# Kernel tuning notes

Hardware: AMD Instinct MI355X
Metric: run time of the kernel (lower is better)

## Reference

```python
import jax, jax.numpy as jnp
from jax import lax
import numpy as np

WIN = 9
PAD = WIN // 2  # 4 -> SAME output size
SIM_FACTOR = 1.0
REG_FACTOR = 0.1
EPS = 1e-5

_DN = ('NCHW', 'OIHW', 'NCHW')


def box_sum(x):
    """9x9 sliding-window sum via two separable 1D ones-convs (same math as a 9x9 ones conv2d)."""
    kh = jnp.ones((1, 1, WIN, 1), x.dtype)
    kw = jnp.ones((1, 1, 1, WIN), x.dtype)
    y = lax.conv_general_dilated(x, kh, (1, 1), [(PAD, PAD), (0, 0)], dimension_numbers=_DN)
    return lax.conv_general_dilated(y, kw, (1, 1), [(0, 0), (PAD, PAD)], dimension_numbers=_DN)


def ncc2d(Ii, Ji):
    win_size = float(WIN * WIN)
    I_sum = box_sum(Ii)
    J_sum = box_sum(Ji)
    I2_sum = box_sum(Ii * Ii)
    J2_sum = box_sum(Ji * Ji)
    IJ_sum = box_sum(Ii * Ji)
    u_I = I_sum / win_size
    u_J = J_sum / win_size
    cross = IJ_sum - u_J * I_sum - u_I * J_sum + u_I * u_J * win_size
    I_var = I2_sum - 2.0 * u_I * I_sum + u_I * u_I * win_size
    J_var = J2_sum - 2.0 * u_J * J_sum + u_J * u_J * win_size
    cc = cross * cross / (I_var * J_var + EPS)
    return -jnp.mean(cc)


def grad2d_l2(y_pred):
    dy = y_pred[:, :, 1:, :] - y_pred[:, :, :-1, :]
    dx = y_pred[:, :, :, 1:] - y_pred[:, :, :, :-1]
    return (jnp.mean(dx * dx) + jnp.mean(dy * dy)) / 2.0


def setup_inputs() -> dict:
    key = jax.random.key(0)
    k1, k2, k3 = jax.random.split(key, 3)
    B, H, W = 64, 512, 512
    return {
        'target_proj': jax.random.uniform(k1, (B, 1, H, W), dtype=jnp.float32),
        'warped_moving': jax.random.uniform(k2, (B, 1, H, W), dtype=jnp.float32),
        'phi': jax.random.normal(k3, (B, 2, H, W), dtype=jnp.float32),
    }


def reference(target_proj, warped_moving, phi):
    loss_sim = ncc2d(target_proj, warped_moving) * SIM_FACTOR
    loss_reg = grad2d_l2(phi) * REG_FACTOR
    total = loss_sim + loss_reg
    return (loss_sim, loss_reg, total)
```

## Files before the change

kernel.cpp:

```cpp
#include <hip/hip_runtime.h>

#define HH 512
#define WW 512
#define RSTRIP 16
#define NCC_BLOCKS 512
#define REG_BLOCKS 512

__device__ __forceinline__ void ldrow8(const float* __restrict__ row, int lane,
                                       float v[8]) {
    const float4* p = reinterpret_cast<const float4*>(row) + (lane << 1);
    float4 a = p[0], b = p[1];
    v[0] = a.x; v[1] = a.y; v[2] = a.z; v[3] = a.w;
    v[4] = b.x; v[5] = b.y; v[6] = b.z; v[7] = b.w;
}

__device__ __forceinline__ void fold(const float d[8], int lane, float* B) {
    float hl0 = __shfl_up(d[4], 1), hl1 = __shfl_up(d[5], 1);
    float hl2 = __shfl_up(d[6], 1), hl3 = __shfl_up(d[7], 1);
    float hr0 = __shfl_down(d[0], 1), hr1 = __shfl_down(d[1], 1);
    float hr2 = __shfl_down(d[2], 1), hr3 = __shfl_down(d[3], 1);
    hl0 = lane ? hl0 : 0.f; hl1 = lane ? hl1 : 0.f;
    hl2 = lane ? hl2 : 0.f; hl3 = lane ? hl3 : 0.f;
    bool nr = (lane != 63);
    hr0 = nr ? hr0 : 0.f; hr1 = nr ? hr1 : 0.f;
    hr2 = nr ? hr2 : 0.f; hr3 = nr ? hr3 : 0.f;

    float s = ((hl0 + hl1) + (hl2 + hl3)) +
              ((d[0] + d[1]) + (d[2] + d[3])) + d[4];
    B[0] += s;
    s += d[5] - hl0;  B[1] += s;
    s += d[6] - hl1;  B[2] += s;
    s += d[7] - hl2;  B[3] += s;
    s += hr0 - hl3;   B[4] += s;
    s += hr1 - d[0];  B[5] += s;
    s += hr2 - d[1];  B[6] += s;
    s += hr3 - d[2];  B[7] += s;
}

template<bool HASL, bool HAST>
__device__ __forceinline__ void upd8(const float* __restrict__ Il,
                                     const float* __restrict__ Jl,
                                     const float* __restrict__ It,
                                     const float* __restrict__ Jt,
                                     int lane, float B[5][8]) {
    float LI[8], LJ[8], TI[8], TJ[8], d[8];
    if (HASL) { ldrow8(Il, lane, LI); ldrow8(Jl, lane, LJ); }
    if (HAST) { ldrow8(It, lane, TI); ldrow8(Jt, lane, TJ); }

#pragma unroll
    for (int c = 0; c < 8; ++c)
        d[c] = HASL ? (HAST ? LI[c] - TI[c] : LI[c]) : -TI[c];
    fold(d, lane, B[0]);
#pragma unroll
    for (int c = 0; c < 8; ++c)
        d[c] = HASL ? (HAST ? LJ[c] - TJ[c] : LJ[c]) : -TJ[c];
    fold(d, lane, B[1]);
#pragma unroll
    for (int c = 0; c < 8; ++c)
        d[c] = HASL ? (HAST ? fmaf(LI[c], LI[c], -(TI[c] * TI[c]))
                            : LI[c] * LI[c])
                    : -(TI[c] * TI[c]);
    fold(d, lane, B[2]);
#pragma unroll
    for (int c = 0; c < 8; ++c)
        d[c] = HASL ? (HAST ? fmaf(LJ[c], LJ[c], -(TJ[c] * TJ[c]))
                            : LJ[c] * LJ[c])
                    : -(TJ[c] * TJ[c]);
    fold(d, lane, B[3]);
#pragma unroll
    for (int c = 0; c < 8; ++c)
        d[c] = HASL ? (HAST ? fmaf(LI[c], LJ[c], -(TI[c] * TJ[c]))
                            : LI[c] * LJ[c])
                    : -(TI[c] * TJ[c]);
    fold(d, lane, B[4]);
}

__device__ void ncc_body(int sbid, const float* __restrict__ I,
                         const float* __restrict__ J, float* __restrict__ ws,
                         float* sh) {
    const int T = threadIdx.x;
    const int lane = T & 63;
    const int strip = (sbid << 2) | (T >> 6);
    const int b = strip >> 5;
    const int s = strip & 31;
    const int r0 = s << 4;

    const float* Ib = I + (size_t)b * (HH * WW);
    const float* Jb = J + (size_t)b * (HH * WW);

    float B[5][8];
#pragma unroll
    for (int k = 0; k < 5; ++k)
#pragma unroll
        for (int o = 0; o < 8; ++o) B[k][o] = 0.f;

    for (int j = r0 - 4; j <= r0 + 4; ++j) {
        if (j >= 0)
            upd8<true, false>(Ib + (size_t)j * WW, Jb + (size_t)j * WW,
                              Ib, Jb, lane, B);
    }

    const float inv81 = 1.f / 81.f;
    float acc = 0.f;
    for (int h = 0;; ++h) {
#pragma unroll
        for (int o = 0; o < 8; ++o) {
            float IS = B[0][o], JS = B[1][o];
            float I2 = B[2][o], J2 = B[3][o], IJ = B[4][o];
            float cross = fmaf(-(IS * JS), inv81, IJ);
            float Iv = fmaf(-(IS * IS), inv81, I2);
            float Jv = fmaf(-(JS * JS), inv81, J2);
            float denom = fmaf(Iv, Jv, 1e-5f);
            acc = fmaf(cross * cross, __builtin_amdgcn_rcpf(denom), acc);
        }
        if (h == RSTRIP - 1) break;
        const int jl = r0 + h + 5;
        const int jt = r0 + h - 4;
        const float* IlP = Ib + (size_t)jl * WW;
        const float* JlP = Jb + (size_t)jl * WW;
        const float* ItP = Ib + (size_t)jt * WW;
        const float* JtP = Jb + (size_t)jt * WW;
        if (jl < HH) {
            if (jt >= 0) upd8<true, true>(IlP, JlP, ItP, JtP, lane, B);
            else         upd8<true, false>(IlP, JlP, Ib, Jb, lane, B);
        } else if (jt >= 0) {
            upd8<false, true>(Ib, Jb, ItP, JtP, lane, B);
        }
    }

#pragma unroll
    for (int off = 32; off; off >>= 1) acc += __shfl_down(acc, off);
    if ((T & 63) == 0) sh[T >> 6] = acc;
    __syncthreads();
    if (T == 0) atomicAdd(&ws[0], sh[0] + sh[1] + sh[2] + sh[3]);
}

__device__ void reg_body(int sbid, const float* __restrict__ P,
                         float* __restrict__ ws, float* sh) {
    const int T = threadIdx.x;
    const int c4 = T & 127;
    const int strip = (sbid << 1) | (T >> 7);
    const size_t row0 = (size_t)strip << 6;
    const bool slast = ((strip & 7) == 7);
    const float* rp = P + row0 * WW + (c4 << 2);

    float sdx = 0.f, sdy = 0.f;
    float4 cur = *reinterpret_cast<const float4*>(rp);
#pragma unroll 8
    for (int i = 0; i < 64; ++i) {
        float d0 = cur.y - cur.x, d1 = cur.z - cur.y, d2 = cur.w - cur.z;
        sdx += d0 * d0 + d1 * d1 + d2 * d2;
        if (c4 < 127) {
            float nx = rp[(size_t)i * WW + 4];
            float d3 = nx - cur.w;
            sdx += d3 * d3;
        }
        if (i < 63) {
            float4 nr = *reinterpret_cast<const float4*>(rp + (size_t)(i + 1) * WW);
            float e0 = nr.x - cur.x, e1 = nr.y - cur.y;
            float e2 = nr.z - cur.z, e3 = nr.w - cur.w;
            sdy += e0 * e0 + e1 * e1 + e2 * e2 + e3 * e3;
            cur = nr;
        } else if (!slast) {
            float4 nr = *reinterpret_cast<const float4*>(rp + (size_t)64 * WW);
            float e0 = nr.x - cur.x, e1 = nr.y - cur.y;
            float e2 = nr.z - cur.z, e3 = nr.w - cur.w;
            sdy += e0 * e0 + e1 * e1 + e2 * e2 + e3 * e3;
        }
    }

#pragma unroll
    for (int off = 32; off; off >>= 1) {
        sdx += __shfl_down(sdx, off);
        sdy += __shfl_down(sdy, off);
    }
    if ((T & 63) == 0) { sh[T >> 6] = sdx; sh[4 + (T >> 6)] = sdy; }
    __syncthreads();
    if (T == 0) {
        atomicAdd(&ws[1], sh[0] + sh[1] + sh[2] + sh[3]);
        atomicAdd(&ws[2], sh[4] + sh[5] + sh[6] + sh[7]);
    }
}

__global__ __launch_bounds__(256) void fused_kernel(const float* __restrict__ I,
                                                    const float* __restrict__ J,
                                                    const float* __restrict__ P,
                                                    float* __restrict__ ws) {
    __shared__ float sh[8];
    const int bid = blockIdx.x;
    if (bid & 1) ncc_body(bid >> 1, I, J, ws, sh);
    else         reg_body(bid >> 1, P, ws, sh);
}

__global__ void finalize_kernel(const float* __restrict__ ws,
                                float* __restrict__ out) {
    float cc_sum = ws[0], dx_sum = ws[1], dy_sum = ws[2];
    float loss_sim = -(cc_sum / 16777216.f);
    float mdx = dx_sum / 33488896.f;
    float mdy = dy_sum / 33488896.f;
    float loss_reg = (mdx + mdy) * 0.5f * 0.1f;
    out[0] = loss_sim;
    out[1] = loss_reg;
    out[2] = loss_sim + loss_reg;
}

extern "C" void kernel_launch(void* const* d_in, const int* in_sizes, int n_in,
                              void* d_out, int out_size, void* d_ws, size_t ws_size,
                              hipStream_t stream) {
    const float* I = (const float*)d_in[0];
    const float* J = (const float*)d_in[1];
    const float* P = (const float*)d_in[2];
    float* out = (float*)d_out;
    float* ws = (float*)d_ws;

    hipMemsetAsync(d_ws, 0, 3 * sizeof(float), stream);
    fused_kernel<<<NCC_BLOCKS + REG_BLOCKS, 256, 0, stream>>>(I, J, P, ws);
    finalize_kernel<<<1, 1, 0, stream>>>(ws, out);
}
```

Baseline: 103.4 us.

## Replace shuffle halos with overlapping 16-wide loads and prefetch leading rows

Each lane now loads 16 columns (its 8 plus 4-column halos on each side) with float4 loads, so the horizontal fold no longer needs cross-lane shuffles. The row loop is unrolled by two with double-buffered leading-row registers, so the next leading row is fetched while the current update is computed. Boundary rows are clamped and zeroed instead of using template branches. This doubles the global/L1 load traffic per row and raises register pressure, which could lower occupancy.

Result: faster. 99.76 us (-3.5%).

```diff
diff --git a/kernel.cpp b/kernel.cpp
--- a/kernel.cpp
+++ b/kernel.cpp
@@ -6,73 +6,97 @@
 #define NCC_BLOCKS 512
 #define REG_BLOCKS 512
 
-__device__ __forceinline__ void ldrow8(const float* __restrict__ row, int lane,
-                                       float v[8]) {
-    const float4* p = reinterpret_cast<const float4*>(row) + (lane << 1);
-    float4 a = p[0], b = p[1];
-    v[0] = a.x; v[1] = a.y; v[2] = a.z; v[3] = a.w;
-    v[4] = b.x; v[5] = b.y; v[6] = b.z; v[7] = b.w;
-}
-
-__device__ __forceinline__ void fold(const float d[8], int lane, float* B) {
-    float hl0 = __shfl_up(d[4], 1), hl1 = __shfl_up(d[5], 1);
-    float hl2 = __shfl_up(d[6], 1), hl3 = __shfl_up(d[7], 1);
-    float hr0 = __shfl_down(d[0], 1), hr1 = __shfl_down(d[1], 1);
-    float hr2 = __shfl_down(d[2], 1), hr3 = __shfl_down(d[3], 1);
-    hl0 = lane ? hl0 : 0.f; hl1 = lane ? hl1 : 0.f;
-    hl2 = lane ? hl2 : 0.f; hl3 = lane ? hl3 : 0.f;
-    bool nr = (lane != 63);
-    hr0 = nr ? hr0 : 0.f; hr1 = nr ? hr1 : 0.f;
-    hr2 = nr ? hr2 : 0.f; hr3 = nr ? hr3 : 0.f;
-
-    float s = ((hl0 + hl1) + (hl2 + hl3)) +
-              ((d[0] + d[1]) + (d[2] + d[3])) + d[4];
+__device__ __forceinline__ void ld16(const float* __restrict__ row, int lane,
+                                     float v[16]) {
+    const float4* p = reinterpret_cast<const float4*>(row);
+    const int b0 = (lane << 1) - 1;
+    float4 a = p[b0 < 0 ? 0 : b0];
+    float4 b = p[b0 + 1];
+    float4 c = p[b0 + 2];
+    float4 e = p[b0 + 3 > 127 ? 127 : b0 + 3];
+    if (b0 < 0)       a = make_float4(0.f, 0.f, 0.f, 0.f);
+    if (b0 + 3 > 127) e = make_float4(0.f, 0.f, 0.f, 0.f);
+    v[0]  = a.x; v[1]  = a.y; v[2]  = a.z; v[3]  = a.w;
+    v[4]  = b.x; v[5]  = b.y; v[6]  = b.z; v[7]  = b.w;
+    v[8]  = c.x; v[9]  = c.y; v[10] = c.z; v[11] = c.w;
+    v[12] = e.x; v[13] = e.y; v[14] = e.z; v[15] = e.w;
+}
+
+__device__ __forceinline__ void ld_rows(const float* __restrict__ Ib,
+                                        const float* __restrict__ Jb,
+                                        int row, int lane,
+                                        float vi[16], float vj[16]) {
+    const int rc = row < 0 ? 0 : (row > HH - 1 ? HH - 1 : row);
+    ld16(Ib + (size_t)rc * WW, lane, vi);
+    ld16(Jb + (size_t)rc * WW, lane, vj);
+    if (rc != row) {
+#pragma unroll
+        for (int i = 0; i < 16; ++i) { vi[i] = 0.f; vj[i] = 0.f; }
+    }
+}
+
+__device__ __forceinline__ void fold16(const float d[16], float* B) {
+    float s = (((d[0] + d[1]) + (d[2] + d[3])) +
+               ((d[4] + d[5]) + (d[6] + d[7]))) + d[8];
     B[0] += s;
-    s += d[5] - hl0;  B[1] += s;
-    s += d[6] - hl1;  B[2] += s;
-    s += d[7] - hl2;  B[3] += s;
-    s += hr0 - hl3;   B[4] += s;
-    s += hr1 - d[0];  B[5] += s;
-    s += hr2 - d[1];  B[6] += s;
-    s += hr3 - d[2];  B[7] += s;
-}
-
-template<bool HASL, bool HAST>
-__device__ __forceinline__ void upd8(const float* __restrict__ Il,
-                                     const float* __restrict__ Jl,
-                                     const float* __restrict__ It,
-                                     const float* __restrict__ Jt,
-                                     int lane, float B[5][8]) {
-    float LI[8], LJ[8], TI[8], TJ[8], d[8];
-    if (HASL) { ldrow8(Il, lane, LI); ldrow8(Jl, lane, LJ); }
-    if (HAST) { ldrow8(It, lane, TI); ldrow8(Jt, lane, TJ); }
-
-#pragma unroll
-    for (int c = 0; c < 8; ++c)
-        d[c] = HASL ? (HAST ? LI[c] - TI[c] : LI[c]) : -TI[c];
-    fold(d, lane, B[0]);
-#pragma unroll
-    for (int c = 0; c < 8; ++c)
-        d[c] = HASL ? (HAST ? LJ[c] - TJ[c] : LJ[c]) : -TJ[c];
-    fold(d, lane, B[1]);
-#pragma unroll
-    for (int c = 0; c < 8; ++c)
-        d[c] = HASL ? (HAST ? fmaf(LI[c], LI[c], -(TI[c] * TI[c]))
-                            : LI[c] * LI[c])
-                    : -(TI[c] * TI[c]);
-    fold(d, lane, B[2]);
-#pragma unroll
-    for (int c = 0; c < 8; ++c)
-        d[c] = HASL ? (HAST ? fmaf(LJ[c], LJ[c], -(TJ[c] * TJ[c]))
-                            : LJ[c] * LJ[c])
-                    : -(TJ[c] * TJ[c]);
-    fold(d, lane, B[3]);
-#pragma unroll
-    for (int c = 0; c < 8; ++c)
-        d[c] = HASL ? (HAST ? fmaf(LI[c], LJ[c], -(TI[c] * TJ[c]))
-                            : LI[c] * LJ[c])
-                    : -(TI[c] * TJ[c]);
-    fold(d, lane, B[4]);
+#pragma unroll
+    for (int o = 1; o < 8; ++o) {
+        s += d[o + 8] - d[o - 1];
+        B[o] += s;
+    }
+}
+
+__device__ __forceinline__ void acc_lead(const float LI[16], const float LJ[16],
+                                         float B[5][8]) {
+    float d[16];
+    fold16(LI, B[0]);
+    fold16(LJ, B[1]);
+#pragma unroll
+    for (int i = 0; i < 16; ++i) d[i] = LI[i] * LI[i];
+    fold16(d, B[2]);
+#pragma unroll
+    for (int i = 0; i < 16; ++i) d[i] = LJ[i] * LJ[i];
+    fold16(d, B[3]);
+#pragma unroll
+    for (int i = 0; i < 16; ++i) d[i] = LI[i] * LJ[i];
+    fold16(d, B[4]);
+}
+
+__device__ __forceinline__ void acc_diff(const float LI[16], const float LJ[16],
+                                         const float TI[16], const float TJ[16],
+                                         float B[5][8]) {
+    float d[16];
+#pragma unroll
+    for (int i = 0; i < 16; ++i) d[i] = LI[i] - TI[i];
+    fold16(d, B[0]);
+#pragma unroll
+    for (int i = 0; i < 16; ++i) d[i] = LJ[i] - TJ[i];
+    fold16(d, B[1]);
+#pragma unroll
+    for (int i = 0; i < 16; ++i) d[i] = fmaf(LI[i], LI[i], -(TI[i] * TI[i]));
+    fold16(d, B[2]);
+#pragma unroll
+    for (int i = 0; i < 16; ++i) d[i] = fmaf(LJ[i], LJ[i], -(TJ[i] * TJ[i]));
+    fold16(d, B[3]);
+#pragma unroll
+    for (int i = 0; i < 16; ++i) d[i] = fmaf(LI[i], LJ[i], -(TI[i] * TJ[i]));
+    fold16(d, B[4]);
+}
+
+__device__ __forceinline__ float cc_row(const float B[5][8]) {
+    const float inv81 = 1.f / 81.f;
+    float a = 0.f;
+#pragma unroll
+    for (int o = 0; o < 8; ++o) {
+        float IS = B[0][o], JS = B[1][o];
+        float I2 = B[2][o], J2 = B[3][o], IJ = B[4][o];
+        float cross = fmaf(-(IS * JS), inv81, IJ);
+        float Iv = fmaf(-(IS * IS), inv81, I2);
+        float Jv = fmaf(-(JS * JS), inv81, J2);
+        float denom = fmaf(Iv, Jv, 1e-5f);
+        a = fmaf(cross * cross, __builtin_amdgcn_rcpf(denom), a);
+    }
+    return a;
 }
 
 __device__ void ncc_body(int sbid, const float* __restrict__ I,
@@ -82,8 +106,7 @@
     const int lane = T & 63;
     const int strip = (sbid << 2) | (T >> 6);
     const int b = strip >> 5;
-    const int s = strip & 31;
-    const int r0 = s << 4;
+    const int r0 = (strip & 31) << 4;
 
     const float* Ib = I + (size_t)b * (HH * WW);
     const float* Jb = J + (size_t)b * (HH * WW);
@@ -94,37 +117,39 @@
 #pragma unroll
         for (int o = 0; o < 8; ++o) B[k][o] = 0.f;
 
-    for (int j = r0 - 4; j <= r0 + 4; ++j) {
-        if (j >= 0)
-            upd8<true, false>(Ib + (size_t)j * WW, Jb + (size_t)j * WW,
-                              Ib, Jb, lane, B);
-    }
-
-    const float inv81 = 1.f / 81.f;
+    {
+        float vi[16], vj[16];
+        for (int j = r0 - 4; j <= r0 + 4; ++j) {
+            if (j >= 0) {
+                ld16(Ib + (size_t)j * WW, lane, vi);
+                ld16(Jb + (size_t)j * WW, lane, vj);
+                acc_lead(vi, vj, B);
+            }
+        }
+    }
+
+    float LAi[16], LAj[16], LBi[16], LBj[16];
+    ld_rows(Ib, Jb, r0 + 5, lane, LAi, LAj);
+
     float acc = 0.f;
-    for (int h = 0;; ++h) {
-#pragma unroll
-        for (int o = 0; o < 8; ++o) {
-            float IS = B[0][o], JS = B[1][o];
-            float I2 = B[2][o], J2 = B[3][o], IJ = B[4][o];
-            float cross = fmaf(-(IS * JS), inv81, IJ);
-            float Iv = fmaf(-(IS * IS), inv81, I2);
-            float Jv = fmaf(-(JS * JS), inv81, J2);
-            float denom = fmaf(Iv, Jv, 1e-5f);
-            acc = fmaf(cross * cross, __builtin_amdgcn_rcpf(denom), acc);
-        }
-        if (h == RSTRIP - 1) break;
-        const int jl = r0 + h + 5;
-        const int jt = r0 + h - 4;
-        const float* IlP = Ib + (size_t)jl * WW;
-        const float* JlP = Jb + (size_t)jl * WW;
-        const float* ItP = Ib + (size_t)jt * WW;
-        const float* JtP = Jb + (size_t)jt * WW;
-        if (jl < HH) {
-            if (jt >= 0) upd8<true, true>(IlP, JlP, ItP, JtP, lane, B);
-            else         upd8<true, false>(IlP, JlP, Ib, Jb, lane, B);
-        } else if (jt >= 0) {
-            upd8<false, true>(Ib, Jb, ItP, JtP, lane, B);
+    for (int k = 0; k < 8; ++k) {
+        {
+            const int h = 2 * k;
+            acc += cc_row(B);
+            float TI[16], TJ[16];
+            ld_rows(Ib, Jb, r0 + h - 4, lane, TI, TJ);
+            ld_rows(Ib, Jb, r0 + h + 6, lane, LBi, LBj);
+            acc_diff(LAi, LAj, TI, TJ, B);
+        }
+        {
+            const int h = 2 * k + 1;
+            acc += cc_row(B);
+            if (h < RSTRIP - 1) {
+                float TI[16], TJ[16];
+                ld_rows(Ib, Jb, r0 + h - 4, lane, TI, TJ);
+                ld_rows(Ib, Jb, r0 + h + 6, lane, LAi, LAj);
+                acc_diff(LBi, LBj, TI, TJ, B);
+            }
         }
     }
 
```
